# Kernel optimization log

Measured on AMD Instinct MI355X. Metric: run time of the kernel, lower is better.

The kernel has to match this reference:

```python
import jax, jax.numpy as jnp
import numpy as np
from jax import lax

B, CIN, COUT, H, W, K, PAD = 8, 64, 64, 256, 256, 3, 1

def setup_inputs() -> dict:
    key = jax.random.key(0)
    k1, k2, k3, k4 = jax.random.split(key, 4)
    x = jax.random.normal(k1, (B, CIN, H, W), dtype=jnp.float32)
    mask = (jax.random.uniform(k2, (B, 1, H, W)) < 0.5).astype(jnp.float32)
    fan_in = CIN * K * K
    bound = 1.0 / np.sqrt(fan_in)
    weight = jax.random.uniform(k3, (COUT, CIN, K, K), minval=-bound, maxval=bound, dtype=jnp.float32)
    bias = jax.random.uniform(k4, (COUT,), minval=-bound, maxval=bound, dtype=jnp.float32)
    return {"x": x, "mask": mask, "weight": weight, "bias": bias}

def _masked_conv(x, mask, weight, bias):
    # Standard conv: the original gathers valid unfold columns, matmuls with the
    # flattened weight + bias, and scatters back; zeros elsewhere. Equivalent to
    # (conv(x) + b) * valid, where valid[b,l] = any(mask patch at l != 0).
    conv = lax.conv_general_dilated(
        x, weight,
        window_strides=(1, 1),
        padding=[(PAD, PAD), (PAD, PAD)],
        dimension_numbers=("NCHW", "OIHW", "NCHW"),
    )
    out = conv + bias[None, :, None, None]
    # any(|mask| != 0) over each KxK window == max-pool of |mask| > 0
    pooled = lax.reduce_window(
        jnp.abs(mask), 0.0, lax.max,
        window_dimensions=(1, 1, K, K),
        window_strides=(1, 1, 1, 1),
        padding=[(0, 0), (0, 0), (PAD, PAD), (PAD, PAD)],
    )
    valid = pooled > 0  # [B,1,H,W], broadcasts over channels
    return jnp.where(valid, out, jnp.zeros((), dtype=out.dtype))

def reference(x, mask, weight, bias):
    return _masked_conv(x, mask, weight, bias)
```

## Files before the change

kernel.cpp:

```cpp
#include <hip/hip_runtime.h>


#define B_    8
#define C_    64
#define H_    256
#define W_    256
#define HW_   (H_ * W_)

typedef __attribute__((ext_vector_type(8))) short bf16x8;
typedef __attribute__((ext_vector_type(4))) float f32x4;

__device__ __forceinline__ unsigned short f2bf(float f) {
    unsigned int u = __float_as_uint(f);
    u = (u + 0x7FFFu + ((u >> 16) & 1u)) >> 16;
    return (unsigned short)u;
}

__global__ __launch_bounds__(256) void wconv(const float* __restrict__ wgt,
                                             unsigned short* __restrict__ wsA)
{
    const int gid  = blockIdx.x * 256 + threadIdx.x;
    const int s    = gid >> 8;
    const int rest = gid & 255;
    const int mf   = rest >> 6;
    const int lane = rest & 63;
    const int tap  = s >> 1;
    const int kblk = s & 1;
    const int kh = tap / 3, kw = tap % 3;
    const int co = mf * 16 + (lane & 15);
    unsigned short v[8];
#pragma unroll
    for (int j = 0; j < 8; ++j) {
        const int ci = kblk * 32 + (lane >> 4) * 8 + j;
        v[j] = f2bf(wgt[((co * C_ + ci) * 3 + kh) * 3 + kw]);
    }
    unsigned short* dst = wsA + (size_t)gid * 8;
    *(uint4*)dst = *(const uint4*)v;
}

#define TROWS 6
#define TCOLS 66
#define CELLP 72

__global__ __launch_bounds__(512, 4) void masked_conv_mfma(
    const float* __restrict__ x,
    const float* __restrict__ mask,
    const unsigned short* __restrict__ wsA,
    const float* __restrict__ bias,
    float* __restrict__ out)
{
    __shared__ unsigned short xs[TROWS * TCOLS * CELLP];

    const int tid  = threadIdx.x;
    const int wave = tid >> 6;
    const int lane = tid & 63;
    const int l15  = lane & 15;
    const int lq   = lane >> 4;

    const int w0 = blockIdx.x * 64;
    const int h0 = blockIdx.y * 4;
    const int b  = blockIdx.z;

    const int NU = TROWS * TCOLS * 8;
    for (int u = tid; u < NU; u += 512) {
        const int col = u % TCOLS;
        const int t2  = u / TCOLS;
        const int oct = t2 & 7;
        const int row = t2 >> 3;
        const int gh = h0 - 1 + row;
        const int gw = w0 - 1 + col;
        unsigned short v[8];
        if (gh >= 0 && gh < H_ && gw >= 0 && gw < W_) {
            const float* px = x + ((size_t)(b * C_ + oct * 8) * H_ + gh) * W_ + gw;
#pragma unroll
            for (int j = 0; j < 8; ++j) v[j] = f2bf(px[(size_t)j * HW_]);
        } else {
#pragma unroll
            for (int j = 0; j < 8; ++j) v[j] = 0;
        }
        *(uint4*)&xs[((row * TCOLS) + col) * CELLP + oct * 8] = *(const uint4*)v;
    }
    __syncthreads();

    const int hrow = wave & 3;
    const int nh   = wave >> 2;

    f32x4 acc[4][2];
#pragma unroll
    for (int mf = 0; mf < 4; ++mf)
#pragma unroll
        for (int nf = 0; nf < 2; ++nf)
            acc[mf][nf] = (f32x4){0.f, 0.f, 0.f, 0.f};

    const bf16x8* wA = (const bf16x8*)wsA;

#pragma unroll 1
    for (int kh = 0; kh < 3; ++kh) {
        const int rowbase = (hrow + kh) * TCOLS + nh * 32;
#pragma unroll
        for (int kw = 0; kw < 3; ++kw) {
#pragma unroll
            for (int kblk = 0; kblk < 2; ++kblk) {
                const int s = (kh * 3 + kw) * 2 + kblk;
                bf16x8 a[4];
#pragma unroll
                for (int mf = 0; mf < 4; ++mf)
                    a[mf] = wA[(s * 4 + mf) * 64 + lane];
                bf16x8 bf[2];
#pragma unroll
                for (int nf = 0; nf < 2; ++nf) {
                    const int cell = rowbase + nf * 16 + l15 + kw;
                    bf[nf] = *(const bf16x8*)&xs[cell * CELLP + kblk * 32 + lq * 8];
                }
#pragma unroll
                for (int mf = 0; mf < 4; ++mf)
#pragma unroll
                    for (int nf = 0; nf < 2; ++nf)
                        acc[mf][nf] = __builtin_amdgcn_mfma_f32_16x16x32_bf16(
                            a[mf], bf[nf], acc[mf][nf], 0, 0, 0);
            }
        }
    }

    const int h = h0 + hrow;
    const int pcol = w0 + nh * 32 + (lane & 31);
    int valid = 0;
    const float* mb = mask + (size_t)b * HW_;
#pragma unroll
    for (int dh = -1; dh <= 1; ++dh) {
        const int hh = h + dh;
        if (hh < 0 || hh >= H_) continue;
#pragma unroll
        for (int dw = -1; dw <= 1; ++dw) {
            const int ww = pcol + dw;
            if (ww < 0 || ww >= W_) continue;
            if (mb[hh * W_ + ww] != 0.0f) valid = 1;
        }
    }

#pragma unroll
    for (int nf = 0; nf < 2; ++nf) {
        const int cloc = nf * 16 + l15;
        const int vn = __builtin_amdgcn_ds_bpermute(cloc << 2, valid);
        float* ob = out + ((size_t)(b * C_) * H_ + h) * W_ + w0 + nh * 32 + cloc;
#pragma unroll
        for (int mf = 0; mf < 4; ++mf) {
#pragma unroll
            for (int reg = 0; reg < 4; ++reg) {
                const int co = mf * 16 + lq * 4 + reg;
                const float val = vn ? (acc[mf][nf][reg] + bias[co]) : 0.0f;
                ob[(size_t)co * HW_] = val;
            }
        }
    }
}

extern "C" void kernel_launch(void* const* d_in, const int* in_sizes, int n_in,
                              void* d_out, int out_size, void* d_ws, size_t ws_size,
                              hipStream_t stream) {
    const float* x    = (const float*)d_in[0];
    const float* mask = (const float*)d_in[1];
    const float* wgt  = (const float*)d_in[2];
    const float* bias = (const float*)d_in[3];
    float* out        = (float*)d_out;
    unsigned short* wsA = (unsigned short*)d_ws;

    wconv<<<18, 256, 0, stream>>>(wgt, wsA);

    dim3 grid(W_ / 64, H_ / 4, B_);
    masked_conv_mfma<<<grid, 512, 0, stream>>>(x, mask, wsA, bias, out);
}
```

Measured before the change: 329.9 us.

## Split input channels into two LDS passes to halve shared memory and raise occupancy

The shared input tile now holds 32 input channels per pass instead of all 64, with two passes over the channel halves. This cuts LDS per block roughly in half, and the launch bounds now request 8 blocks per CU instead of 4. Global loads for each pass are issued ahead of the bf16 conversion and LDS stores to give some overlap. The mask-validity check and its lane permutes now run before the main loop, hiding their latency. The cost is an extra barrier and tile fill per block, plus possible register pressure under the tighter launch bound.

New measurement: 337.4 us. +2.3%, slower.

```diff
diff --git a/kernel.cpp b/kernel.cpp
--- a/kernel.cpp
+++ b/kernel.cpp
@@ -40,16 +40,18 @@
 
 #define TROWS 6
 #define TCOLS 66
-#define CELLP 72
+#define CELLP 40
+#define NU2   (TROWS * TCOLS * 4)
+#define NTAIL (NU2 - 3 * 512)
 
-__global__ __launch_bounds__(512, 4) void masked_conv_mfma(
+__global__ __launch_bounds__(512, 8) void masked_conv_mfma(
     const float* __restrict__ x,
     const float* __restrict__ mask,
     const unsigned short* __restrict__ wsA,
     const float* __restrict__ bias,
     float* __restrict__ out)
 {
-    __shared__ unsigned short xs[TROWS * TCOLS * CELLP];
+    __shared__ __align__(16) unsigned short xs[TROWS * TCOLS * CELLP];
 
     const int tid  = threadIdx.x;
     const int wave = tid >> 6;
@@ -61,29 +63,30 @@
     const int h0 = blockIdx.y * 4;
     const int b  = blockIdx.z;
 
-    const int NU = TROWS * TCOLS * 8;
-    for (int u = tid; u < NU; u += 512) {
-        const int col = u % TCOLS;
-        const int t2  = u / TCOLS;
-        const int oct = t2 & 7;
-        const int row = t2 >> 3;
-        const int gh = h0 - 1 + row;
-        const int gw = w0 - 1 + col;
-        unsigned short v[8];
-        if (gh >= 0 && gh < H_ && gw >= 0 && gw < W_) {
-            const float* px = x + ((size_t)(b * C_ + oct * 8) * H_ + gh) * W_ + gw;
-#pragma unroll
-            for (int j = 0; j < 8; ++j) v[j] = f2bf(px[(size_t)j * HW_]);
-        } else {
-#pragma unroll
-            for (int j = 0; j < 8; ++j) v[j] = 0;
-        }
-        *(uint4*)&xs[((row * TCOLS) + col) * CELLP + oct * 8] = *(const uint4*)v;
-    }
-    __syncthreads();
+    const float* xb = x + (size_t)b * C_ * HW_;
 
     const int hrow = wave & 3;
     const int nh   = wave >> 2;
+    const int h    = h0 + hrow;
+    const int pcol = w0 + nh * 32 + (lane & 31);
+
+    int valid = 0;
+    {
+        const float* mb = mask + (size_t)b * HW_;
+#pragma unroll
+        for (int dh = -1; dh <= 1; ++dh) {
+#pragma unroll
+            for (int dw = -1; dw <= 1; ++dw) {
+                const int hh = h + dh;
+                const int ww = pcol + dw;
+                const int ok = (hh >= 0) & (hh < H_) & (ww >= 0) & (ww < W_);
+                const float mv = mb[ok ? (hh * W_ + ww) : 0];
+                valid |= ok & (mv != 0.0f ? 1 : 0);
+            }
+        }
+    }
+    const int vn0 = __builtin_amdgcn_ds_bpermute(l15 << 2, valid);
+    const int vn1 = __builtin_amdgcn_ds_bpermute((16 + l15) << 2, valid);
 
     f32x4 acc[4][2];
 #pragma unroll
@@ -95,53 +98,74 @@
     const bf16x8* wA = (const bf16x8*)wsA;
 
 #pragma unroll 1
-    for (int kh = 0; kh < 3; ++kh) {
-        const int rowbase = (hrow + kh) * TCOLS + nh * 32;
+    for (int p = 0; p < 2; ++p) {
+        float va0[8], va1[8];
+        int   cl0, cl1, ok0, ok1;
+
+        auto issue = [&](int k, float (&va)[8], int& cl, int& ok) {
+            const int u   = tid + (k << 9);
+            const int col = u % TCOLS;
+            const int t2  = u / TCOLS;
+            const int oct2 = t2 & 3;
+            const int row  = t2 >> 2;
+            const int gh = h0 - 1 + row;
+            const int gw = w0 - 1 + col;
+            ok = (gh >= 0) & (gh < H_) & (gw >= 0) & (gw < W_);
+            const float* px = xb + ((size_t)((p * 4 + oct2) * 8) * H_
+                                    + (ok ? gh : 0)) * W_ + (ok ? gw : 0);
 #pragma unroll
-        for (int kw = 0; kw < 3; ++kw) {
+            for (int j = 0; j < 8; ++j) va[j] = px[(size_t)j * HW_];
+            cl = (row * TCOLS + col) * CELLP + oct2 * 8;
+        };
+        auto wr = [&](const float (&va)[8], int cl, int ok) {
+            unsigned short v[8];
 #pragma unroll
-            for (int kblk = 0; kblk < 2; ++kblk) {
-                const int s = (kh * 3 + kw) * 2 + kblk;
+            for (int j = 0; j < 8; ++j)
+                v[j] = ok ? f2bf(va[j]) : (unsigned short)0;
+            *(uint4*)&xs[cl] = *(const uint4*)v;
+        };
+
+        issue(0, va0, cl0, ok0);
+        issue(1, va1, cl1, ok1);
+        if (p) __syncthreads();
+        wr(va0, cl0, ok0);
+        issue(2, va0, cl0, ok0);
+        wr(va1, cl1, ok1);
+        if (tid < NTAIL) issue(3, va1, cl1, ok1);
+        wr(va0, cl0, ok0);
+        if (tid < NTAIL) wr(va1, cl1, ok1);
+        __syncthreads();
+
+#pragma unroll 1
+        for (int kh = 0; kh < 3; ++kh) {
+            const int rowbase = (hrow + kh) * TCOLS + nh * 32;
+#pragma unroll
+            for (int kw = 0; kw < 3; ++kw) {
+                const int s = (kh * 3 + kw) * 2 + p;
                 bf16x8 a[4];
 #pragma unroll
                 for (int mf = 0; mf < 4; ++mf)
                     a[mf] = wA[(s * 4 + mf) * 64 + lane];
-                bf16x8 bf[2];
+                bf16x8 bfv[2];
 #pragma unroll
                 for (int nf = 0; nf < 2; ++nf) {
-                    const int cell = rowbase + nf * 16 + l15 + kw;
-                    bf[nf] = *(const bf16x8*)&xs[cell * CELLP + kblk * 32 + lq * 8];
+                    const int cell2 = rowbase + nf * 16 + l15 + kw;
+                    bfv[nf] = *(const bf16x8*)&xs[cell2 * CELLP + lq * 8];
                 }
 #pragma unroll
                 for (int mf = 0; mf < 4; ++mf)
 #pragma unroll
                     for (int nf = 0; nf < 2; ++nf)
                         acc[mf][nf] = __builtin_amdgcn_mfma_f32_16x16x32_bf16(
-                            a[mf], bf[nf], acc[mf][nf], 0, 0, 0);
+                            a[mf], bfv[nf], acc[mf][nf], 0, 0, 0);
             }
-        }
-    }
-
-    const int h = h0 + hrow;
-    const int pcol = w0 + nh * 32 + (lane & 31);
-    int valid = 0;
-    const float* mb = mask + (size_t)b * HW_;
-#pragma unroll
-    for (int dh = -1; dh <= 1; ++dh) {
-        const int hh = h + dh;
-        if (hh < 0 || hh >= H_) continue;
-#pragma unroll
-        for (int dw = -1; dw <= 1; ++dw) {
-            const int ww = pcol + dw;
-            if (ww < 0 || ww >= W_) continue;
-            if (mb[hh * W_ + ww] != 0.0f) valid = 1;
         }
     }
 
 #pragma unroll
     for (int nf = 0; nf < 2; ++nf) {
         const int cloc = nf * 16 + l15;
-        const int vn = __builtin_amdgcn_ds_bpermute(cloc << 2, valid);
+        const int vn = nf ? vn1 : vn0;
         float* ob = out + ((size_t)(b * C_) * H_ + h) * W_ + w0 + nh * 32 + cloc;
 #pragma unroll
         for (int mf = 0; mf < 4; ++mf) {
```
